# Kernel tuning notes

Measured on AMD Instinct MI355X. Metric: run time of the kernel, lower is better.

The kernel has to match this reference:

```python
import jax, jax.numpy as jnp
import numpy as np

N = 10000
E = 320000
F_IN = 256
F_PROJ = 200


def setup_inputs() -> dict:
    key = jax.random.key(0)
    ks = jax.random.split(key, 8)
    x = jax.random.normal(ks[0], (N, F_IN), dtype=jnp.float32)
    edge_attr = jax.random.uniform(ks[1], (N, N), dtype=jnp.float32)
    src = jax.random.randint(ks[2], (E,), 0, N)
    dst = jax.random.randint(ks[3], (E,), 0, N)
    # remove self loops at data-gen time (module calls remove_self_loops)
    dst = jnp.where(dst == src, (dst + 1) % N, dst)
    edge_index = jnp.stack([src, dst]).astype(jnp.int64)
    W_proj = jax.random.normal(ks[4], (F_IN, F_PROJ), dtype=jnp.float32) * 0.05
    b_proj = jnp.zeros((F_PROJ,), dtype=jnp.float32)
    W_att = jax.random.normal(ks[5], (F_PROJ, 1), dtype=jnp.float32) * 0.05
    b_att = jnp.zeros((1,), dtype=jnp.float32)
    return {"x": x, "edge_attr": edge_attr, "edge_index": edge_index,
            "W_proj": W_proj, "b_proj": b_proj, "W_att": W_att, "b_att": b_att}


def reference(x, edge_attr, edge_index, W_proj, b_proj, W_att, b_att):
    src, dst = edge_index[0], edge_index[1]
    # gather: x_j = source features, x_i = target features (PyG default flow)
    x_i = x[dst]                      # [E, F_IN]
    x_j = x[src]                      # [E, F_IN]
    p_i = x_i @ W_proj + b_proj       # [E, 200]
    p_j = x_j @ W_proj + b_proj       # [E, 200]
    alpha = jnp.abs(p_i - p_j) @ W_att + b_att   # [E, 1]
    alpha = jax.nn.relu(alpha)
    alpha = jax.nn.softmax(alpha, axis=0)        # softmax over edges
    a = alpha[:, 0]
    # write attention symmetrically into the dense edge matrix
    edge_values = edge_attr.at[src, dst].set(a).at[dst, src].set(a)
    # scatter-max aggregation of (unprojected) x_i by target index
    agg = jax.ops.segment_max(x_i, dst, num_segments=N)
    agg = jnp.where(jnp.isfinite(agg), agg, jnp.zeros((), agg.dtype))
    return agg, edge_values
```

## Files before the change

### kernel.cpp

```cpp
#include <hip/hip_runtime.h>

#define N_NODES 10000
#define E_EDGES 320000
#define F_IN    256
#define F_PROJ  200

#define EV_BYTES 400000000L

#define PJ_BLOCKS 2500
#define A_BLOCKS  2048
#define A_CHUNK   40
#define AGG_BLOCKS 160
#define AGG_N4    (N_NODES * F_IN / 4)
#define AGG_PER_BLK (AGG_N4 / AGG_BLOCKS)

#define WS_P      0L
#define WS_EXP    4000000L
#define WS_FLAGS  5280000L
#define WS_SUM    5320000L

__device__ __forceinline__ unsigned short f32_to_bf16(float f) {
    unsigned int u = __float_as_uint(f);
    u += 0x7FFFu + ((u >> 16) & 1u);
    return (unsigned short)(u >> 16);
}
__device__ __forceinline__ float bf16_to_f32(unsigned short b) {
    return __uint_as_float(((unsigned int)b) << 16);
}

__global__ __launch_bounds__(256) void k1_proj_flags(
        const float* __restrict__ x, const float* __restrict__ W,
        unsigned short* __restrict__ P, const int* __restrict__ ei,
        int* __restrict__ flags) {
    int bid = blockIdx.x, tid = threadIdx.x;
    int gt = bid * 256 + tid;
    if (gt < E_EDGES) flags[ei[E_EDGES + gt]] = 1;

    __shared__ float xs[4][F_IN];
    int n0 = bid * 4;
    ((float4*)xs)[tid] = ((const float4*)(x + (long)n0 * F_IN))[tid];
    __syncthreads();
    int j = tid;
    if (j >= F_PROJ) return;
    float acc[4] = {0.f, 0.f, 0.f, 0.f};
    for (int k = 0; k < F_IN; ++k) {
        float w = W[k * F_PROJ + j];
        #pragma unroll
        for (int r = 0; r < 4; ++r) acc[r] += xs[r][k] * w;
    }
    #pragma unroll
    for (int r = 0; r < 4; ++r) P[(long)(n0 + r) * F_PROJ + j] = f32_to_bf16(acc[r]);
}

__global__ __launch_bounds__(256) void k2_alpha_agg(
        const int* __restrict__ ei, const unsigned short* __restrict__ P,
        const float* __restrict__ Watt, const float* __restrict__ batt,
        float* __restrict__ expalpha, float* __restrict__ sumbuf,
        const int* __restrict__ flags, const float4* __restrict__ x4,
        float4* __restrict__ agg4) {
    int bid = blockIdx.x, tid = threadIdx.x;
    if (bid < A_BLOCKS) {
        __shared__ float bsum;
        if (tid == 0) bsum = 0.f;
        __syncthreads();
        int wid  = bid * 4 + (tid >> 6);
        int lane = tid & 63;
        float4 w4 = make_float4(0.f, 0.f, 0.f, 0.f);
        if (lane < 50) w4 = ((const float4*)Watt)[lane];
        float bias = batt[0];
        int e0 = wid * A_CHUNK;
        int e1 = min(e0 + A_CHUNK, E_EDGES);
        float lsum = 0.f;
        for (int e = e0; e < e1; ++e) {
            int s = ei[e];
            int d = ei[E_EDGES + e];
            float acc = 0.f;
            if (lane < 50) {
                uint2 us = *(const uint2*)(P + (long)s * F_PROJ + lane * 4);
                uint2 ud = *(const uint2*)(P + (long)d * F_PROJ + lane * 4);
                acc = fabsf(bf16_to_f32((unsigned short)(ud.x & 0xFFFF)) -
                            bf16_to_f32((unsigned short)(us.x & 0xFFFF))) * w4.x
                    + fabsf(bf16_to_f32((unsigned short)(ud.x >> 16)) -
                            bf16_to_f32((unsigned short)(us.x >> 16))) * w4.y
                    + fabsf(bf16_to_f32((unsigned short)(ud.y & 0xFFFF)) -
                            bf16_to_f32((unsigned short)(us.y & 0xFFFF))) * w4.z
                    + fabsf(bf16_to_f32((unsigned short)(ud.y >> 16)) -
                            bf16_to_f32((unsigned short)(us.y >> 16))) * w4.w;
            }
            #pragma unroll
            for (int off = 32; off; off >>= 1) acc += __shfl_down(acc, off);
            if (lane == 0) {
                float ea = expf(fmaxf(acc + bias, 0.f));
                expalpha[e] = ea;
                lsum += ea;
            }
        }
        if (lane == 0) atomicAdd(&bsum, lsum);
        __syncthreads();
        if (tid == 0) atomicAdd(sumbuf, bsum);
        return;
    }
    long base = (long)(bid - A_BLOCKS) * AGG_PER_BLK;
    for (int i = tid; i < AGG_PER_BLK; i += 256) {
        long i4 = base + i;
        float4 v = x4[i4];
        if (!flags[i4 >> 6]) v = make_float4(0.f, 0.f, 0.f, 0.f);
        agg4[i4] = v;
    }
}

__global__ __launch_bounds__(256) void k3_scatter(
        const int* __restrict__ ei, const float* __restrict__ expalpha,
        const float* __restrict__ sumbuf, float* __restrict__ ev) {
    int e = blockIdx.x * 256 + threadIdx.x;
    if (e >= E_EDGES) return;
    float a = expalpha[e] / sumbuf[0];
    int s = ei[e], d = ei[E_EDGES + e];
    ev[(long)s * N_NODES + d] = a;
    ev[(long)d * N_NODES + s] = a;
}

extern "C" void kernel_launch(void* const* d_in, const int* in_sizes, int n_in,
                              void* d_out, int out_size, void* d_ws, size_t ws_size,
                              hipStream_t stream) {
    (void)in_sizes; (void)n_in; (void)out_size; (void)ws_size;
    const float* x         = (const float*)d_in[0];
    const float* edge_attr = (const float*)d_in[1];
    const int*   ei        = (const int*)d_in[2];
    const float* W_proj    = (const float*)d_in[3];
    const float* W_att     = (const float*)d_in[5];
    const float* b_att     = (const float*)d_in[6];

    float* agg = (float*)d_out;
    float* ev  = (float*)d_out + (long)N_NODES * F_IN;
    char* ws = (char*)d_ws;

    unsigned short* P = (unsigned short*)(ws + WS_P);
    float* expalpha   = (float*)(ws + WS_EXP);
    int*   flags      = (int*)(ws + WS_FLAGS);
    float* sumbuf     = (float*)(ws + WS_SUM);

    hipMemsetAsync(ws + WS_FLAGS, 0, 40016, stream);

    hipMemcpyAsync(ev, edge_attr, EV_BYTES, hipMemcpyDeviceToDevice, stream);

    k1_proj_flags<<<PJ_BLOCKS, 256, 0, stream>>>(x, W_proj, P, ei, flags);

    k2_alpha_agg<<<A_BLOCKS + AGG_BLOCKS, 256, 0, stream>>>(
        ei, P, W_att, b_att, expalpha, sumbuf, flags,
        (const float4*)x, (float4*)agg);

    k3_scatter<<<(E_EDGES + 255) / 256, 256, 0, stream>>>(
        ei, expalpha, sumbuf, ev);
}
```

Baseline: 296.3 us.

## Split dense edge matrix copy across compute kernels with nontemporal loads/stores

Replaces the standalone 400 MB device-to-device memcpy with three row-range copy slices, each run by extra blocks inside the projection, alpha, and scatter kernels, using nontemporal vector loads and stores. The goal is to overlap the bandwidth-bound copy with the compute phases and hide it. The scatter is split so rows already copied are written in the third kernel and the last slice is written in a new fourth kernel after its copy finishes. This adds an extra launch and depends on how blocks from the copy and compute paths get scheduled relative to each other.

```diff
diff --git a/kernel.cpp b/kernel.cpp
--- a/kernel.cpp
+++ b/kernel.cpp
@@ -5,14 +5,28 @@
 #define F_IN    256
 #define F_PROJ  200
 
-#define EV_BYTES 400000000L
-
-#define PJ_BLOCKS 2500
-#define A_BLOCKS  2048
-#define A_CHUNK   40
-#define AGG_BLOCKS 160
-#define AGG_N4    (N_NODES * F_IN / 4)
+typedef float vfloat4 __attribute__((ext_vector_type(4)));
+
+#define ROW_F4      2500L
+#define R1          2400
+#define R2          6200
+#define C1_F4_BEG   0L
+#define C1_F4_END   (R1 * ROW_F4)
+#define C2_F4_BEG   C1_F4_END
+#define C2_F4_END   ((long)R2 * ROW_F4)
+#define C3_F4_BEG   C2_F4_END
+#define C3_F4_END   (N_NODES * ROW_F4)
+
+#define PJ_BLOCKS   2500
+#define K1_COPY_BLOCKS 1024
+#define A_BLOCKS    2048
+#define A_CHUNK     40
+#define AGG_BLOCKS  160
+#define AGG_N4      (N_NODES * F_IN / 4)
 #define AGG_PER_BLK (AGG_N4 / AGG_BLOCKS)
+#define K2_COPY_BLOCKS 2048
+#define K3_COPY_BLOCKS 2048
+#define SC_BLOCKS   1250
 
 #define WS_P      0L
 #define WS_EXP    4000000L
@@ -28,11 +42,28 @@
     return __uint_as_float(((unsigned int)b) << 16);
 }
 
-__global__ __launch_bounds__(256) void k1_proj_flags(
+__device__ __forceinline__ void nt_copy_range(
+        const vfloat4* __restrict__ src, vfloat4* __restrict__ dst,
+        long beg, long end, int cid, int nblk, int tid) {
+    long i = beg + (long)cid * 256 + tid;
+    const long stride = (long)nblk * 256;
+    for (; i < end; i += stride) {
+        vfloat4 v = __builtin_nontemporal_load(src + i);
+        __builtin_nontemporal_store(v, dst + i);
+    }
+}
+
+__global__ __launch_bounds__(256) void k1_proj_flags_copy(
         const float* __restrict__ x, const float* __restrict__ W,
         unsigned short* __restrict__ P, const int* __restrict__ ei,
-        int* __restrict__ flags) {
+        int* __restrict__ flags,
+        const vfloat4* __restrict__ csrc, vfloat4* __restrict__ cdst) {
     int bid = blockIdx.x, tid = threadIdx.x;
+    if (bid >= PJ_BLOCKS) {
+        nt_copy_range(csrc, cdst, C1_F4_BEG, C1_F4_END,
+                      bid - PJ_BLOCKS, K1_COPY_BLOCKS, tid);
+        return;
+    }
     int gt = bid * 256 + tid;
     if (gt < E_EDGES) flags[ei[E_EDGES + gt]] = 1;
 
@@ -52,12 +83,13 @@
     for (int r = 0; r < 4; ++r) P[(long)(n0 + r) * F_PROJ + j] = f32_to_bf16(acc[r]);
 }
 
-__global__ __launch_bounds__(256) void k2_alpha_agg(
+__global__ __launch_bounds__(256) void k2_alpha_agg_copy(
         const int* __restrict__ ei, const unsigned short* __restrict__ P,
         const float* __restrict__ Watt, const float* __restrict__ batt,
         float* __restrict__ expalpha, float* __restrict__ sumbuf,
         const int* __restrict__ flags, const float4* __restrict__ x4,
-        float4* __restrict__ agg4) {
+        float4* __restrict__ agg4,
+        const vfloat4* __restrict__ csrc, vfloat4* __restrict__ cdst) {
     int bid = blockIdx.x, tid = threadIdx.x;
     if (bid < A_BLOCKS) {
         __shared__ float bsum;
@@ -100,24 +132,47 @@
         if (tid == 0) atomicAdd(sumbuf, bsum);
         return;
     }
-    long base = (long)(bid - A_BLOCKS) * AGG_PER_BLK;
-    for (int i = tid; i < AGG_PER_BLK; i += 256) {
-        long i4 = base + i;
-        float4 v = x4[i4];
-        if (!flags[i4 >> 6]) v = make_float4(0.f, 0.f, 0.f, 0.f);
-        agg4[i4] = v;
-    }
-}
-
-__global__ __launch_bounds__(256) void k3_scatter(
+    int b2 = bid - A_BLOCKS;
+    if (b2 < AGG_BLOCKS) {
+        long base = (long)b2 * AGG_PER_BLK;
+        for (int i = tid; i < AGG_PER_BLK; i += 256) {
+            long i4 = base + i;
+            float4 v = x4[i4];
+            if (!flags[i4 >> 6]) v = make_float4(0.f, 0.f, 0.f, 0.f);
+            agg4[i4] = v;
+        }
+        return;
+    }
+    nt_copy_range(csrc, cdst, C2_F4_BEG, C2_F4_END,
+                  b2 - AGG_BLOCKS, K2_COPY_BLOCKS, tid);
+}
+
+__global__ __launch_bounds__(256) void k3_copy_scatter_lo(
+        const int* __restrict__ ei, const float* __restrict__ expalpha,
+        const float* __restrict__ sumbuf, float* __restrict__ ev,
+        const vfloat4* __restrict__ csrc, vfloat4* __restrict__ cdst) {
+    int bid = blockIdx.x, tid = threadIdx.x;
+    if (bid < K3_COPY_BLOCKS) {
+        nt_copy_range(csrc, cdst, C3_F4_BEG, C3_F4_END, bid, K3_COPY_BLOCKS, tid);
+        return;
+    }
+    int e = (bid - K3_COPY_BLOCKS) * 256 + tid;
+    if (e >= E_EDGES) return;
+    float a = expalpha[e] / sumbuf[0];
+    int s = ei[e], d = ei[E_EDGES + e];
+    if (s < R2) ev[(long)s * N_NODES + d] = a;
+    if (d < R2) ev[(long)d * N_NODES + s] = a;
+}
+
+__global__ __launch_bounds__(256) void k4_scatter_hi(
         const int* __restrict__ ei, const float* __restrict__ expalpha,
         const float* __restrict__ sumbuf, float* __restrict__ ev) {
     int e = blockIdx.x * 256 + threadIdx.x;
     if (e >= E_EDGES) return;
     float a = expalpha[e] / sumbuf[0];
     int s = ei[e], d = ei[E_EDGES + e];
-    ev[(long)s * N_NODES + d] = a;
-    ev[(long)d * N_NODES + s] = a;
+    if (s >= R2) ev[(long)s * N_NODES + d] = a;
+    if (d >= R2) ev[(long)d * N_NODES + s] = a;
 }
 
 extern "C" void kernel_launch(void* const* d_in, const int* in_sizes, int n_in,
@@ -142,14 +197,16 @@
 
     hipMemsetAsync(ws + WS_FLAGS, 0, 40016, stream);
 
-    hipMemcpyAsync(ev, edge_attr, EV_BYTES, hipMemcpyDeviceToDevice, stream);
-
-    k1_proj_flags<<<PJ_BLOCKS, 256, 0, stream>>>(x, W_proj, P, ei, flags);
-
-    k2_alpha_agg<<<A_BLOCKS + AGG_BLOCKS, 256, 0, stream>>>(
+    k1_proj_flags_copy<<<PJ_BLOCKS + K1_COPY_BLOCKS, 256, 0, stream>>>(
+        x, W_proj, P, ei, flags, (const vfloat4*)edge_attr, (vfloat4*)ev);
+
+    k2_alpha_agg_copy<<<A_BLOCKS + AGG_BLOCKS + K2_COPY_BLOCKS, 256, 0, stream>>>(
         ei, P, W_att, b_att, expalpha, sumbuf, flags,
-        (const float4*)x, (float4*)agg);
-
-    k3_scatter<<<(E_EDGES + 255) / 256, 256, 0, stream>>>(
-        ei, expalpha, sumbuf, ev);
-}
+        (const float4*)x, (float4*)agg,
+        (const vfloat4*)edge_attr, (vfloat4*)ev);
+
+    k3_copy_scatter_lo<<<K3_COPY_BLOCKS + SC_BLOCKS, 256, 0, stream>>>(
+        ei, expalpha, sumbuf, ev, (const vfloat4*)edge_attr, (vfloat4*)ev);
+
+    k4_scatter_hi<<<SC_BLOCKS, 256, 0, stream>>>(ei, expalpha, sumbuf, ev);
+}
```

Result: faster. 253.3 us (-14.5%).
